# Optimization experiments

Measured on AMD Instinct MI355X. Metric: run time of the kernel, lower is better.

Reference implementation:

```python
import jax, jax.numpy as jnp
import numpy as np

DIM = 4096
N_HEADS = 32
HEAD_DIM = DIM // N_HEADS
BSZ = 4
SEQLEN = 512
MAX_SEQ = 2048
NEG = -1e9


def _qlinear(x, q, s):
    # int-quantized weight [out,in] dequantized with per-output-channel scale
    w = q.astype(jnp.float32) * s[:, None]
    return jnp.einsum('bsd,od->bso', x, w)


def _apply_rotary(xq, xk, cos, sin):
    # xq,xk: [b,s,h,hd]; cos,sin: [s,hd/2]
    def rot(t):
        b, s, h, d = t.shape
        t = t.reshape(b, s, h, d // 2, 2)
        tr, ti = t[..., 0], t[..., 1]
        c = cos[None, :, None, :]
        sn = sin[None, :, None, :]
        out_r = tr * c - ti * sn
        out_i = tr * sn + ti * c
        return jnp.stack([out_r, out_i], axis=-1).reshape(b, s, h, d)
    return rot(xq), rot(xk)


def setup_inputs() -> dict:
    key = jax.random.key(0)
    ks = jax.random.split(key, 12)
    x = jax.random.normal(ks[0], (BSZ, SEQLEN, DIM), dtype=jnp.float32)
    inv = 1.0 / (10000.0 ** (jnp.arange(0, HEAD_DIM, 2, dtype=jnp.float32) / HEAD_DIM))
    ang = jnp.arange(SEQLEN, dtype=jnp.float32)[:, None] * inv[None, :]
    freqs_cos, freqs_sin = jnp.cos(ang), jnp.sin(ang)
    input_idexes = jnp.arange(SEQLEN, dtype=jnp.int32)  # cache slots being written
    # causal additive mask over full cache: query at position i may attend j <= i
    j = jnp.arange(MAX_SEQ)
    mask = jnp.where(j[None, :] <= input_idexes[:, None], 0.0, NEG).astype(jnp.float32)
    mask = mask[None, None]  # [1,1,S,MAX_SEQ]
    cache_k = jnp.zeros((BSZ, MAX_SEQ, N_HEADS, HEAD_DIM), jnp.float32)
    cache_v = jnp.zeros((BSZ, MAX_SEQ, N_HEADS, HEAD_DIM), jnp.float32)
    SCALE = 2.0 / (127.0 * np.sqrt(DIM))
    def mkw(kq, kscale):
        q = jax.random.randint(kq, (DIM, DIM), -127, 128, dtype=jnp.int32)
        s = jax.random.uniform(kscale, (DIM,), dtype=jnp.float32) * SCALE
        return q, s
    wq_q, wq_s = mkw(ks[1], ks[2])
    wk_q, wk_s = mkw(ks[3], ks[4])
    wv_q, wv_s = mkw(ks[5], ks[6])
    wo_q, wo_s = mkw(ks[7], ks[8])
    return dict(x=x, freqs_cos=freqs_cos, freqs_sin=freqs_sin, mask=mask,
                input_idexes=input_idexes, cache_k=cache_k, cache_v=cache_v,
                wq_q=wq_q, wq_s=wq_s, wk_q=wk_q, wk_s=wk_s,
                wv_q=wv_q, wv_s=wv_s, wo_q=wo_q, wo_s=wo_s)


def reference(x, freqs_cos, freqs_sin, mask, input_idexes, cache_k, cache_v,
              wq_q, wq_s, wk_q, wk_s, wv_q, wv_s, wo_q, wo_s):
    bsz, seqlen, _ = x.shape
    xq = _qlinear(x, wq_q, wq_s).reshape(bsz, seqlen, N_HEADS, HEAD_DIM)
    xk = _qlinear(x, wk_q, wk_s).reshape(bsz, seqlen, N_HEADS, HEAD_DIM)
    xv = _qlinear(x, wv_q, wv_s).reshape(bsz, seqlen, N_HEADS, HEAD_DIM)
    xq, xk = _apply_rotary(xq, xk, freqs_cos, freqs_sin)
    # KV-cache append (index_copy on dim 1)
    cache_k = cache_k.at[:, input_idexes].set(xk)
    cache_v = cache_v.at[:, input_idexes].set(xv)
    # [b,h,q,d] x [b,h,k,d] -> [b,h,q,k]
    scores = jnp.einsum('bqhd,bkhd->bhqk', xq, cache_k) / np.sqrt(HEAD_DIM)
    scores = scores + mask
    probs = jax.nn.softmax(scores.astype(jnp.float32), axis=-1).astype(xq.dtype)
    out = jnp.einsum('bhqk,bkhd->bqhd', probs, cache_v).reshape(bsz, seqlen, -1)
    out = _qlinear(out, wo_q, wo_s)
    return out, (cache_k, cache_v)
```

## Files before the change

### kernel.cpp

```cpp
#include <hip/hip_runtime.h>
#include <cstdint>
#include <cstddef>

typedef __bf16 bf16;
typedef __attribute__((ext_vector_type(8))) __bf16 bf16x8;
typedef __attribute__((ext_vector_type(2))) __bf16 bf16x2;
typedef __attribute__((ext_vector_type(4))) float f32x4;
typedef __attribute__((ext_vector_type(2))) float f32x2;
typedef __attribute__((ext_vector_type(4))) int i32x4;

#define DIMN 4096
#define SEQ 512
#define MAXSEQ 2048
#define NHEAD 32
#define HD 128
#define NBH 128
#define MTOK 2048

#define BM 128
#define BN 128
#define BK 32
#define BKI 128

__device__ __forceinline__ void gld_lds16(const void* g, void* l) {
  __builtin_amdgcn_global_load_lds(
      (const __attribute__((address_space(1))) unsigned int*)g,
      (__attribute__((address_space(3))) unsigned int*)l, 16, 0, 0);
}

__device__ __forceinline__ void gemm_core(const bf16* Ablk, const bf16* Bblk,
                                          int lda, int ldb, int kmax,
                                          f32x4 acc[4][4], bf16* As, bf16* Bs) {
  const int tid = threadIdx.x;
  const int wave = tid >> 6;
  const int lane = tid & 63;
  const int wm = (wave >> 1) * 64;
  const int wn = (wave & 1) * 64;
  const int lrow = lane & 15;
  const int lkq8 = (lane >> 4) * 8;
  const int srow = wave * 32 + (lane >> 2);
  const int scol = (lane & 3) * 8;
  const bf16* Ag = Ablk + (size_t)srow * lda + scol;
  const bf16* Bg = Bblk + (size_t)srow * ldb + scol;
  bf16* lA = As + wave * 32 * BK;
  bf16* lB = Bs + wave * 32 * BK;

  for (int k0 = 0; k0 < kmax; k0 += BK) {
    __syncthreads();
    gld_lds16(Ag + k0, lA);
    gld_lds16(Ag + k0 + (size_t)16 * lda, lA + 16 * BK);
    gld_lds16(Bg + k0, lB);
    gld_lds16(Bg + k0 + (size_t)16 * ldb, lB + 16 * BK);
    __syncthreads();
    bf16x8 a[4], b[4];
#pragma unroll
    for (int i = 0; i < 4; ++i)
      a[i] = *(const bf16x8*)(As + (wm + i * 16 + lrow) * BK + lkq8);
#pragma unroll
    for (int i = 0; i < 4; ++i)
      b[i] = *(const bf16x8*)(Bs + (wn + i * 16 + lrow) * BK + lkq8);
#pragma unroll
    for (int mi = 0; mi < 4; ++mi)
#pragma unroll
      for (int ni = 0; ni < 4; ++ni)
        acc[mi][ni] = __builtin_amdgcn_mfma_f32_16x16x32_bf16(a[mi], b[ni], acc[mi][ni], 0, 0, 0);
  }
}

__device__ __forceinline__ void gemm_core_i8(const char* Ablk, const char* Bblk,
                                             int lda, int ldb, int kmax,
                                             i32x4 acc[4][4], char* As, char* Bs) {
  const int tid = threadIdx.x;
  const int wave = tid >> 6;
  const int lane = tid & 63;
  const int wm = (wave >> 1) * 64;
  const int wn = (wave & 1) * 64;
  const int lrow = lane & 15;
  const int q = lane >> 4;
  const int srow = wave * 32 + (lane >> 3);
  const int scol = (((lane & 7) ^ ((lane >> 3) & 7)) * 16);
  const char* Ag = Ablk + (size_t)srow * lda + scol;
  const char* Bg = Bblk + (size_t)srow * ldb + scol;
  char* lA = As + wave * 32 * BKI;
  char* lB = Bs + wave * 32 * BKI;

  for (int k0 = 0; k0 < kmax; k0 += BKI) {
    __syncthreads();
#pragma unroll
    for (int r = 0; r < 4; ++r) {
      gld_lds16(Ag + k0 + (size_t)(8 * r) * lda, lA + 8 * r * BKI);
      gld_lds16(Bg + k0 + (size_t)(8 * r) * ldb, lB + 8 * r * BKI);
    }
    __syncthreads();
#pragma unroll
    for (int kk = 0; kk < 2; ++kk) {
      i32x4 a[4], b[4];
#pragma unroll
      for (int i = 0; i < 4; ++i) {
        const int row = wm + i * 16 + lrow;
        const int slot = (kk * 4 + q) ^ (lrow & 7);
        a[i] = *(const i32x4*)(As + row * BKI + slot * 16);
      }
#pragma unroll
      for (int i = 0; i < 4; ++i) {
        const int row = wn + i * 16 + lrow;
        const int slot = (kk * 4 + q) ^ (lrow & 7);
        b[i] = *(const i32x4*)(Bs + row * BKI + slot * 16);
      }
#pragma unroll
      for (int mi = 0; mi < 4; ++mi)
#pragma unroll
        for (int ni = 0; ni < 4; ++ni)
          acc[mi][ni] = __builtin_amdgcn_mfma_i32_16x16x64_i8(a[mi], b[ni], acc[mi][ni], 0, 0, 0);
    }
  }
}

#define ACC_INIT_F(acc)                                 \
  f32x4 acc[4][4];                                      \
  _Pragma("unroll") for (int _i = 0; _i < 4; ++_i)      \
      _Pragma("unroll") for (int _j = 0; _j < 4; ++_j)  \
          acc[_i][_j] = f32x4{0.f, 0.f, 0.f, 0.f};

#define ACC_INIT_I(acc)                                 \
  i32x4 acc[4][4];                                      \
  _Pragma("unroll") for (int _i = 0; _i < 4; ++_i)      \
      _Pragma("unroll") for (int _j = 0; _j < 4; ++_j)  \
          acc[_i][_j] = i32x4{0, 0, 0, 0};

#define EPI_COORDS                                      \
  const int lane = threadIdx.x & 63;                    \
  const int wave = threadIdx.x >> 6;                    \
  const int wm = (wave >> 1) * 64, wn = (wave & 1) * 64;\
  const int cq = (lane >> 4) * 4, cc = lane & 15;

__global__ __launch_bounds__(256) void k_prep(
    const int* __restrict__ q0, const int* __restrict__ q1,
    const int* __restrict__ q2, const int* __restrict__ q3,
    char* __restrict__ w8, const float* __restrict__ x,
    char* __restrict__ x8, float* __restrict__ xs,
    float* __restrict__ ck, float* __restrict__ cv) {
  __shared__ float red[4];
  const int bx = blockIdx.x;
  const int tid = threadIdx.x;
  if (bx < 16384) {
    const int w = bx >> 12;
    const int* q = (w == 0) ? q0 : (w == 1) ? q1 : (w == 2) ? q2 : q3;
    char* wp = w8 + (size_t)w * 16777216ull;
    size_t i = ((size_t)(bx & 4095) * 256 + tid) * 16;
    const i32x4* qp = (const i32x4*)(q + i);
    i32x4 a = qp[0], b = qp[1], c = qp[2], d = qp[3];
    i32x4 o;
    o[0] = (a[0] & 255) | ((a[1] & 255) << 8) | ((a[2] & 255) << 16) | (a[3] << 24);
    o[1] = (b[0] & 255) | ((b[1] & 255) << 8) | ((b[2] & 255) << 16) | (b[3] << 24);
    o[2] = (c[0] & 255) | ((c[1] & 255) << 8) | ((c[2] & 255) << 16) | (c[3] << 24);
    o[3] = (d[0] & 255) | ((d[1] & 255) << 8) | ((d[2] & 255) << 16) | (d[3] << 24);
    *(i32x4*)(wp + i) = o;
  } else if (bx < 18432) {
    const int row = bx - 16384;
    const float* src = x + (size_t)row * DIMN + tid * 16;
    f32x4 v[4];
#pragma unroll
    for (int j = 0; j < 4; ++j) v[j] = ((const f32x4*)src)[j];
    float am = 0.f;
#pragma unroll
    for (int j = 0; j < 4; ++j)
#pragma unroll
      for (int e = 0; e < 4; ++e) am = fmaxf(am, fabsf(v[j][e]));
#pragma unroll
    for (int off = 32; off; off >>= 1) am = fmaxf(am, __shfl_xor(am, off, 64));
    if ((tid & 63) == 0) red[tid >> 6] = am;
    __syncthreads();
    am = fmaxf(fmaxf(red[0], red[1]), fmaxf(red[2], red[3]));
    const float inv = am > 0.f ? 127.f / am : 0.f;
    i32x4 o;
#pragma unroll
    for (int j = 0; j < 4; ++j) {
      int b0 = (int)rintf(v[j][0] * inv), b1 = (int)rintf(v[j][1] * inv);
      int b2 = (int)rintf(v[j][2] * inv), b3 = (int)rintf(v[j][3] * inv);
      o[j] = (b0 & 255) | ((b1 & 255) << 8) | ((b2 & 255) << 16) | (b3 << 24);
    }
    *(i32x4*)(x8 + (size_t)row * DIMN + tid * 16) = o;
    if (tid == 0) xs[row] = am * (1.f / 127.f);
  } else {
    const int z = bx - 18432;
    const int region = z / 6144;
    const int zoff = z - region * 6144;
    const int b = region >> 1;
    float* base = (region & 1) ? cv : ck;
    char* p = (char*)(base + ((size_t)b * MAXSEQ + SEQ) * DIMN);
    *(f32x4*)(p + (size_t)zoff * 4096 + tid * 16) = f32x4{0.f, 0.f, 0.f, 0.f};
  }
}

__global__ __launch_bounds__(256) void k_quant_attn(const bf16* __restrict__ at,
                                                    char* __restrict__ a8,
                                                    float* __restrict__ as_) {
  __shared__ float red[4];
  const int row = blockIdx.x, tid = threadIdx.x;
  const bf16* src = at + (size_t)row * DIMN + tid * 16;
  bf16x8 h0 = ((const bf16x8*)src)[0], h1 = ((const bf16x8*)src)[1];
  float f[16];
#pragma unroll
  for (int j = 0; j < 8; ++j) { f[j] = (float)h0[j]; f[8 + j] = (float)h1[j]; }
  float am = 0.f;
#pragma unroll
  for (int j = 0; j < 16; ++j) am = fmaxf(am, fabsf(f[j]));
#pragma unroll
  for (int off = 32; off; off >>= 1) am = fmaxf(am, __shfl_xor(am, off, 64));
  if ((tid & 63) == 0) red[tid >> 6] = am;
  __syncthreads();
  am = fmaxf(fmaxf(red[0], red[1]), fmaxf(red[2], red[3]));
  const float inv = am > 0.f ? 127.f / am : 0.f;
  i32x4 o;
#pragma unroll
  for (int j = 0; j < 4; ++j) {
    int b0 = (int)rintf(f[j * 4 + 0] * inv), b1 = (int)rintf(f[j * 4 + 1] * inv);
    int b2 = (int)rintf(f[j * 4 + 2] * inv), b3 = (int)rintf(f[j * 4 + 3] * inv);
    o[j] = (b0 & 255) | ((b1 & 255) << 8) | ((b2 & 255) << 16) | (b3 << 24);
  }
  *(i32x4*)(a8 + (size_t)row * DIMN + tid * 16) = o;
  if (tid == 0) as_[row] = am * (1.f / 127.f);
}

__global__ __launch_bounds__(256, 2) void k_gemm_qkv8(
    const char* __restrict__ X8, const char* __restrict__ W8,
    const float* __restrict__ xs, const float* __restrict__ sq,
    const float* __restrict__ sk, const float* __restrict__ sv,
    const float* __restrict__ fc, const float* __restrict__ fs,
    const int* __restrict__ idx, bf16* __restrict__ qbf,
    bf16* __restrict__ kbf, float* __restrict__ ck, float* __restrict__ cv) {
  __shared__ __align__(16) char As[BM * BKI];
  __shared__ __align__(16) char Bs[BN * BKI];
  const int n0 = blockIdx.x * BN;
  const int m0 = blockIdx.y * BM;
  const int z = blockIdx.z;
  const char* W = W8 + (size_t)z * 16777216ull;
  const float* sw = (z == 0) ? sq : (z == 1) ? sk : sv;
  ACC_INIT_I(acc);
  gemm_core_i8(X8 + (size_t)m0 * DIMN, W + (size_t)n0 * DIMN, DIMN, DIMN, DIMN, acc, As, Bs);
  EPI_COORDS;
  if (z < 2) {
    bf16* dst = (z == 0) ? qbf : kbf;
#pragma unroll
    for (int mi = 0; mi < 4; ++mi)
#pragma unroll
      for (int ni = 0; ni < 4; ++ni)
#pragma unroll
        for (int r = 0; r < 4; ++r) {
          const int row = m0 + wm + mi * 16 + cq + r;
          const int col = n0 + wn + ni * 16 + cc;
          const float v = (float)acc[mi][ni][r] * xs[row] * sw[col];
          const float pv = __shfl_xor(v, 1, 64);
          const int s = row & 511, b = row >> 9;
          const int hd = col & 127, h = col >> 7;
          const int d2 = hd >> 1;
          const float c = fc[s * 64 + d2], sn = fs[s * 64 + d2];
          const float o = (col & 1) ? (pv * sn + v * c) : (v * c - pv * sn);
          dst[(((size_t)(b * NHEAD + h)) * SEQ + s) * HD + hd] = (bf16)o;
          if (z == 1) {
            const int pos = idx[s];
            ck[((size_t)b * MAXSEQ + pos) * DIMN + col] = o;
          }
        }
  } else {
#pragma unroll
    for (int mi = 0; mi < 4; ++mi)
#pragma unroll
      for (int ni = 0; ni < 4; ++ni)
#pragma unroll
        for (int r = 0; r < 4; ++r) {
          const int row = m0 + wm + mi * 16 + cq + r;
          const int col = n0 + wn + ni * 16 + cc;
          const int s = row & 511, b = row >> 9;
          cv[((size_t)b * MAXSEQ + s) * DIMN + col] =
              (float)acc[mi][ni][r] * xs[row] * sw[col];
        }
  }
}

__global__ __launch_bounds__(256) void k_vt(const float* __restrict__ cv,
                                            bf16* __restrict__ vt) {
  __shared__ float tile[32][129];
  const int s0 = blockIdx.x * 32;
  const int bh = blockIdx.y;
  const int b = bh >> 5, h = bh & 31;
  const int tid = threadIdx.x;
  const float* src = cv + (size_t)b * MAXSEQ * DIMN + h * HD;
#pragma unroll
  for (int p = 0; p < 16; ++p) {
    const int row = p * 2 + (tid >> 7);
    const int d = tid & 127;
    tile[row][d] = src[(size_t)(s0 + row) * DIMN + d];
  }
  __syncthreads();
  bf16* dst = vt + (size_t)bh * HD * SEQ;
#pragma unroll
  for (int c = 0; c < 16; ++c) {
    const int d = c * 8 + (tid >> 5);
    const int sl = tid & 31;
    dst[(size_t)d * SEQ + s0 + sl] = (bf16)tile[sl][d];
  }
}

__constant__ int g_tm[10] = {0, 1, 1, 2, 2, 2, 3, 3, 3, 3};
__constant__ int g_tn[10] = {0, 0, 1, 0, 1, 2, 0, 1, 2, 3};

__global__ __launch_bounds__(256, 2) void k_gemm_qk(
    const bf16* __restrict__ qb, const bf16* __restrict__ kb,
    bf16* __restrict__ sc) {
  const int m0 = g_tm[blockIdx.x] * BM;
  const int n0 = g_tn[blockIdx.x] * BN;
  const int bh = blockIdx.z;
  __shared__ __align__(16) bf16 As[BM * BK];
  __shared__ __align__(16) bf16 Bs[BN * BK];
  ACC_INIT_F(acc);
  gemm_core(qb + (size_t)bh * SEQ * HD + (size_t)m0 * HD,
            kb + (size_t)bh * SEQ * HD + (size_t)n0 * HD, HD, HD, HD, acc, As, Bs);
  EPI_COORDS;
  bf16* dst = sc + (size_t)bh * SEQ * SEQ;
#pragma unroll
  for (int mi = 0; mi < 4; ++mi)
#pragma unroll
    for (int ni = 0; ni < 4; ++ni)
#pragma unroll
      for (int r = 0; r < 4; ++r) {
        const int row = m0 + wm + mi * 16 + cq + r;
        const int col = n0 + wn + ni * 16 + cc;
        dst[(size_t)row * SEQ + col] = (bf16)(acc[mi][ni][r] * 0.08838834764831845f);
      }
}

__global__ __launch_bounds__(256) void k_softmax(bf16* __restrict__ sc) {
  const int row = blockIdx.x * 4 + (threadIdx.x >> 6);
  const int lane = threadIdx.x & 63;
  const int q = row & 511;
  bf16* p = sc + (size_t)row * SEQ + lane * 8;
  bf16x8 v8 = *(const bf16x8*)p;
  float lv[8];
  float m = -3.0e38f;
#pragma unroll
  for (int j = 0; j < 8; ++j) {
    const int kj = lane * 8 + j;
    lv[j] = (kj <= q) ? (float)v8[j] : -3.0e38f;
    m = fmaxf(m, lv[j]);
  }
#pragma unroll
  for (int off = 32; off; off >>= 1) m = fmaxf(m, __shfl_xor(m, off, 64));
  float e[8];
  float sum = 0.f;
#pragma unroll
  for (int j = 0; j < 8; ++j) {
    e[j] = (lane * 8 + j <= q) ? __expf(lv[j] - m) : 0.f;
    sum += e[j];
  }
#pragma unroll
  for (int off = 32; off; off >>= 1) sum += __shfl_xor(sum, off, 64);
  const float r = 1.f / sum;
  bf16x8 o;
#pragma unroll
  for (int j = 0; j < 8; ++j) o[j] = (bf16)(e[j] * r);
  *(bf16x8*)p = o;
}

__global__ __launch_bounds__(256, 2) void k_gemm_pv(
    const bf16* __restrict__ P, const bf16* __restrict__ vt,
    bf16* __restrict__ attn) {
  const int m0 = blockIdx.y * BM;
  const int bh = blockIdx.z;
  const int kmax = m0 + BM;
  __shared__ __align__(16) bf16 As[BM * BK];
  __shared__ __align__(16) bf16 Bs[BN * BK];
  ACC_INIT_F(acc);
  gemm_core(P + (size_t)bh * SEQ * SEQ + (size_t)m0 * SEQ,
            vt + (size_t)bh * HD * SEQ, SEQ, SEQ, kmax, acc, As, Bs);
  EPI_COORDS;
  const int b = bh >> 5, h = bh & 31;
#pragma unroll
  for (int mi = 0; mi < 4; ++mi)
#pragma unroll
    for (int ni = 0; ni < 4; ++ni)
#pragma unroll
      for (int r = 0; r < 4; ++r) {
        const int row = m0 + wm + mi * 16 + cq + r;
        const int col = wn + ni * 16 + cc;
        attn[((size_t)(b * SEQ + row)) * DIMN + h * HD + col] = (bf16)acc[mi][ni][r];
      }
}

__global__ __launch_bounds__(256, 2) void k_gemm_out8(
    const char* __restrict__ A8, const char* __restrict__ WO8,
    const float* __restrict__ as_, const float* __restrict__ so,
    float* __restrict__ out) {
  __shared__ __align__(16) char As[BM * BKI];
  __shared__ __align__(16) char Bs[BN * BKI];
  const int n0 = blockIdx.x * BN;
  const int m0 = blockIdx.y * BM;
  ACC_INIT_I(acc);
  gemm_core_i8(A8 + (size_t)m0 * DIMN, WO8 + (size_t)n0 * DIMN, DIMN, DIMN, DIMN, acc, As, Bs);
  EPI_COORDS;
#pragma unroll
  for (int mi = 0; mi < 4; ++mi)
#pragma unroll
    for (int ni = 0; ni < 4; ++ni)
#pragma unroll
      for (int r = 0; r < 4; ++r) {
        const int row = m0 + wm + mi * 16 + cq + r;
        const int col = n0 + wn + ni * 16 + cc;
        out[(size_t)row * DIMN + col] = (float)acc[mi][ni][r] * as_[row] * so[col];
      }
}

extern "C" void kernel_launch(void* const* d_in, const int* in_sizes, int n_in,
                              void* d_out, int out_size, void* d_ws, size_t ws_size,
                              hipStream_t stream) {
  const float* x = (const float*)d_in[0];
  const float* fc = (const float*)d_in[1];
  const float* fs = (const float*)d_in[2];
  const int* idx = (const int*)d_in[4];
  const int* wq_q = (const int*)d_in[7];
  const int* wk_q = (const int*)d_in[9];
  const int* wv_q = (const int*)d_in[11];
  const int* wo_q = (const int*)d_in[13];
  const float* wq_s = (const float*)d_in[8];
  const float* wk_s = (const float*)d_in[10];
  const float* wv_s = (const float*)d_in[12];
  const float* wo_s = (const float*)d_in[14];

  float* out = (float*)d_out;
  float* ck_out = out + 8388608;
  float* cv_out = ck_out + 33554432;

  char* ws = (char*)d_ws;
  char* W8   = ws;
  char* X8   = ws + 67108864ull;
  float* XS  = (float*)(ws + 75497472ull);
  float* AS  = (float*)(ws + 75513856ull);
  bf16* QBF  = (bf16*)(ws + 83886080ull);
  bf16* KBF  = (bf16*)(ws + 100663296ull);
  bf16* VTB  = (bf16*)(ws + 117440512ull);
  bf16* ATTN = (bf16*)(ws + 134217728ull);
  char* A8   = ws + 150994944ull;
  bf16* SC   = (bf16*)(ws + 167772160ull);

  k_prep<<<dim3(67584), 256, 0, stream>>>(wq_q, wk_q, wv_q, wo_q, W8, x, X8, XS,
                                          ck_out, cv_out);
  k_gemm_qkv8<<<dim3(32, 16, 3), 256, 0, stream>>>(
      X8, W8, XS, wq_s, wk_s, wv_s, fc, fs, idx, QBF, KBF, ck_out, cv_out);
  k_vt<<<dim3(16, 128), 256, 0, stream>>>(cv_out, VTB);
  k_gemm_qk<<<dim3(10, 1, 128), 256, 0, stream>>>(QBF, KBF, SC);
  k_softmax<<<dim3(16384), 256, 0, stream>>>(SC);
  k_gemm_pv<<<dim3(1, 4, 128), 256, 0, stream>>>(SC, VTB, ATTN);
  k_quant_attn<<<dim3(2048), 256, 0, stream>>>(ATTN, A8, AS);
  k_gemm_out8<<<dim3(32, 16), 256, 0, stream>>>(A8, W8 + 50331648ull, AS, wo_s, out);
  (void)in_sizes; (void)n_in; (void)out_size; (void)ws_size;
}
```

Baseline: 871.9 us.

## Rewrite int8 GEMM core as 256x256 double-buffered pipelined tile with 8 waves

Replaces the 128x128 int8 GEMM core with a 256x256 block tile run by 512 threads, using a 128KB double-buffered LDS layout with a swizzle. Global-to-LDS loads for the next k-tiles are interleaved with MFMA groups, separated by explicit barriers, scheduler barriers, waitcnt and setprio hints. The aim is to hide load latency and raise operand reuse per block in both the QKV and output projections. In exchange the grids shrink to 384 and 128 blocks, which may leave CUs idle, especially for the output projection. The pipeline also prefetches k-tiles past the end of each row.

```diff
diff --git a/kernel.cpp b/kernel.cpp
--- a/kernel.cpp
+++ b/kernel.cpp
@@ -20,7 +20,6 @@
 #define BM 128
 #define BN 128
 #define BK 32
-#define BKI 128
 
 __device__ __forceinline__ void gld_lds16(const void* g, void* l) {
   __builtin_amdgcn_global_load_lds(
@@ -67,52 +66,92 @@
   }
 }
 
-__device__ __forceinline__ void gemm_core_i8(const char* Ablk, const char* Bblk,
-                                             int lda, int ldb, int kmax,
-                                             i32x4 acc[4][4], char* As, char* Bs) {
+
+#define PBAR do {                              \
+    asm volatile("" ::: "memory");             \
+    __builtin_amdgcn_sched_barrier(0);         \
+    __builtin_amdgcn_s_barrier();              \
+    __builtin_amdgcn_sched_barrier(0);         \
+    asm volatile("" ::: "memory");             \
+  } while (0)
+
+#define STG_A(KT, H, LB) do {                                    \
+    const char* _g = Asrc + (KT) * 128 + (H) * 64;               \
+    char* _l = (LB) + (H) * 16384 + sdst;                        \
+    gld_lds16(_g, _l);                                           \
+    gld_lds16(_g + (size_t)128 * DIMN, _l + 8192);               \
+  } while (0)
+#define STG_B(KT, H, LB) do {                                    \
+    const char* _g = Bsrc + (KT) * 128 + (H) * 64;               \
+    char* _l = (LB) + 32768 + (H) * 16384 + sdst;                \
+    gld_lds16(_g, _l);                                           \
+    gld_lds16(_g + (size_t)128 * DIMN, _l + 8192);               \
+  } while (0)
+
+#define LDA8(DST, MI, H, LB) \
+  DST = *(const i32x4*)((LB) + (H) * 16384 + (MI) * 1024 + aoff)
+#define LDB8(DST, NI, H, LB) \
+  DST = *(const i32x4*)((LB) + (H) * 16384 + (NI) * 1024 + boff)
+
+#define MFMA16(G)                                                           \
+    __builtin_amdgcn_s_setprio(1);                                          \
+    _Pragma("unroll") for (int _i = 0; _i < 4; ++_i)                        \
+      _Pragma("unroll") for (int _n = 0; _n < 4; ++_n)                      \
+        acc[(G) * 4 + _i][_n] = __builtin_amdgcn_mfma_i32_16x16x64_i8(      \
+            a[_i], b[_n], acc[(G) * 4 + _i][_n], 0, 0, 0);                  \
+    __builtin_amdgcn_s_setprio(0)
+
+#define TILE8(T, CUR, OTH) do {                                             \
+    i32x4 a[4], b[4];                                                       \
+                                              \
+    _Pragma("unroll") for (int n = 0; n < 4; ++n) LDB8(b[n], n, 0, CUR);    \
+    _Pragma("unroll") for (int i = 0; i < 4; ++i) LDA8(a[i], i, 0, CUR);    \
+    STG_A((T) + 1, 1, OTH);                                                 \
+    PBAR; MFMA16(0); PBAR;                                                  \
+                                              \
+    _Pragma("unroll") for (int i = 0; i < 4; ++i) LDA8(a[i], 4 + i, 0, CUR);\
+    STG_B((T) + 1, 1, OTH);                                                 \
+    PBAR; MFMA16(1); PBAR;                                                  \
+                                              \
+    _Pragma("unroll") for (int n = 0; n < 4; ++n) LDB8(b[n], n, 1, CUR);    \
+    _Pragma("unroll") for (int i = 0; i < 4; ++i) LDA8(a[i], i, 1, CUR);    \
+    STG_A((T) + 2, 0, CUR);                                                 \
+    PBAR; MFMA16(0); PBAR;                                                  \
+                                              \
+    _Pragma("unroll") for (int i = 0; i < 4; ++i) LDA8(a[i], 4 + i, 1, CUR);\
+    STG_B((T) + 2, 0, CUR);                                                 \
+    asm volatile("s_waitcnt vmcnt(4)" ::: "memory");                        \
+    PBAR; MFMA16(1); PBAR;                                                  \
+  } while (0)
+
+__device__ __forceinline__ void gemm256_i8(const char* __restrict__ Ablk,
+                                           const char* __restrict__ Bblk,
+                                           char* lds, i32x4 acc[8][4]) {
   const int tid = threadIdx.x;
-  const int wave = tid >> 6;
-  const int lane = tid & 63;
-  const int wm = (wave >> 1) * 64;
-  const int wn = (wave & 1) * 64;
-  const int lrow = lane & 15;
-  const int q = lane >> 4;
-  const int srow = wave * 32 + (lane >> 3);
-  const int scol = (((lane & 7) ^ ((lane >> 3) & 7)) * 16);
-  const char* Ag = Ablk + (size_t)srow * lda + scol;
-  const char* Bg = Bblk + (size_t)srow * ldb + scol;
-  char* lA = As + wave * 32 * BKI;
-  char* lB = Bs + wave * 32 * BKI;
-
-  for (int k0 = 0; k0 < kmax; k0 += BKI) {
-    __syncthreads();
-#pragma unroll
-    for (int r = 0; r < 4; ++r) {
-      gld_lds16(Ag + k0 + (size_t)(8 * r) * lda, lA + 8 * r * BKI);
-      gld_lds16(Bg + k0 + (size_t)(8 * r) * ldb, lB + 8 * r * BKI);
-    }
-    __syncthreads();
-#pragma unroll
-    for (int kk = 0; kk < 2; ++kk) {
-      i32x4 a[4], b[4];
-#pragma unroll
-      for (int i = 0; i < 4; ++i) {
-        const int row = wm + i * 16 + lrow;
-        const int slot = (kk * 4 + q) ^ (lrow & 7);
-        a[i] = *(const i32x4*)(As + row * BKI + slot * 16);
-      }
-#pragma unroll
-      for (int i = 0; i < 4; ++i) {
-        const int row = wn + i * 16 + lrow;
-        const int slot = (kk * 4 + q) ^ (lrow & 7);
-        b[i] = *(const i32x4*)(Bs + row * BKI + slot * 16);
-      }
-#pragma unroll
-      for (int mi = 0; mi < 4; ++mi)
-#pragma unroll
-        for (int ni = 0; ni < 4; ++ni)
-          acc[mi][ni] = __builtin_amdgcn_mfma_i32_16x16x64_i8(a[mi], b[ni], acc[mi][ni], 0, 0, 0);
-    }
+  const int wave = tid >> 6, lane = tid & 63;
+  const int wm = (wave >> 2) * 128, wn = (wave & 3) * 64;
+  const int lrow = lane & 15, q = lane >> 4;
+  const int swz = ((q ^ (lrow & 3)) << 4);
+  const int aoff = (wm + lrow) * 64 + swz;
+  const int boff = 32768 + (wn + lrow) * 64 + swz;
+  const int gsw = ((lane & 3) ^ ((lane >> 2) & 3)) << 4;
+  const char* Asrc = Ablk + (size_t)(wave * 16 + (lane >> 2)) * DIMN + gsw;
+  const char* Bsrc = Bblk + (size_t)(wave * 16 + (lane >> 2)) * DIMN + gsw;
+  const int sdst = wave * 1024;
+  char* const L0 = lds;
+  char* const L1 = lds + 65536;
+
+  STG_A(0, 0, L0); STG_B(0, 0, L0);
+  STG_A(0, 1, L0); STG_B(0, 1, L0);
+  STG_A(1, 0, L1); STG_B(1, 0, L1);
+  asm volatile("s_waitcnt vmcnt(4)" ::: "memory");
+  __builtin_amdgcn_sched_barrier(0);
+  __builtin_amdgcn_s_barrier();
+  __builtin_amdgcn_sched_barrier(0);
+
+  for (int t = 0; t < DIMN / 128; t += 2) {
+    TILE8(t, L0, L1);
+    TILE8(t + 1, L1, L0);
   }
 }
 
@@ -122,9 +161,9 @@
       _Pragma("unroll") for (int _j = 0; _j < 4; ++_j)  \
           acc[_i][_j] = f32x4{0.f, 0.f, 0.f, 0.f};
 
-#define ACC_INIT_I(acc)                                 \
-  i32x4 acc[4][4];                                      \
-  _Pragma("unroll") for (int _i = 0; _i < 4; ++_i)      \
+#define ACC_INIT_I8(acc)                                \
+  i32x4 acc[8][4];                                      \
+  _Pragma("unroll") for (int _i = 0; _i < 8; ++_i)      \
       _Pragma("unroll") for (int _j = 0; _j < 4; ++_j)  \
           acc[_i][_j] = i32x4{0, 0, 0, 0};
 
@@ -132,6 +171,12 @@
   const int lane = threadIdx.x & 63;                    \
   const int wave = threadIdx.x >> 6;                    \
   const int wm = (wave >> 1) * 64, wn = (wave & 1) * 64;\
+  const int cq = (lane >> 4) * 4, cc = lane & 15;
+
+#define EPI8_COORDS                                       \
+  const int lane = threadIdx.x & 63;                      \
+  const int wave = threadIdx.x >> 6;                      \
+  const int wm = (wave >> 2) * 128, wn = (wave & 3) * 64; \
   const int cq = (lane >> 4) * 4, cc = lane & 15;
 
 __global__ __launch_bounds__(256) void k_prep(
@@ -223,27 +268,26 @@
   if (tid == 0) as_[row] = am * (1.f / 127.f);
 }
 
-__global__ __launch_bounds__(256, 2) void k_gemm_qkv8(
+__global__ __launch_bounds__(512, 2) void k_gemm_qkv8(
     const char* __restrict__ X8, const char* __restrict__ W8,
     const float* __restrict__ xs, const float* __restrict__ sq,
     const float* __restrict__ sk, const float* __restrict__ sv,
     const float* __restrict__ fc, const float* __restrict__ fs,
     const int* __restrict__ idx, bf16* __restrict__ qbf,
     bf16* __restrict__ kbf, float* __restrict__ ck, float* __restrict__ cv) {
-  __shared__ __align__(16) char As[BM * BKI];
-  __shared__ __align__(16) char Bs[BN * BKI];
-  const int n0 = blockIdx.x * BN;
-  const int m0 = blockIdx.y * BM;
+  __shared__ __align__(16) char lds[131072];
+  const int n0 = blockIdx.x * 256;
+  const int m0 = blockIdx.y * 256;
   const int z = blockIdx.z;
   const char* W = W8 + (size_t)z * 16777216ull;
   const float* sw = (z == 0) ? sq : (z == 1) ? sk : sv;
-  ACC_INIT_I(acc);
-  gemm_core_i8(X8 + (size_t)m0 * DIMN, W + (size_t)n0 * DIMN, DIMN, DIMN, DIMN, acc, As, Bs);
-  EPI_COORDS;
+  ACC_INIT_I8(acc);
+  gemm256_i8(X8 + (size_t)m0 * DIMN, W + (size_t)n0 * DIMN, lds, acc);
+  EPI8_COORDS;
   if (z < 2) {
     bf16* dst = (z == 0) ? qbf : kbf;
 #pragma unroll
-    for (int mi = 0; mi < 4; ++mi)
+    for (int mi = 0; mi < 8; ++mi)
 #pragma unroll
       for (int ni = 0; ni < 4; ++ni)
 #pragma unroll
@@ -265,7 +309,7 @@
         }
   } else {
 #pragma unroll
-    for (int mi = 0; mi < 4; ++mi)
+    for (int mi = 0; mi < 8; ++mi)
 #pragma unroll
       for (int ni = 0; ni < 4; ++ni)
 #pragma unroll
@@ -388,19 +432,18 @@
       }
 }
 
-__global__ __launch_bounds__(256, 2) void k_gemm_out8(
+__global__ __launch_bounds__(512, 2) void k_gemm_out8(
     const char* __restrict__ A8, const char* __restrict__ WO8,
     const float* __restrict__ as_, const float* __restrict__ so,
     float* __restrict__ out) {
-  __shared__ __align__(16) char As[BM * BKI];
-  __shared__ __align__(16) char Bs[BN * BKI];
-  const int n0 = blockIdx.x * BN;
-  const int m0 = blockIdx.y * BM;
-  ACC_INIT_I(acc);
-  gemm_core_i8(A8 + (size_t)m0 * DIMN, WO8 + (size_t)n0 * DIMN, DIMN, DIMN, DIMN, acc, As, Bs);
-  EPI_COORDS;
-#pragma unroll
-  for (int mi = 0; mi < 4; ++mi)
+  __shared__ __align__(16) char lds[131072];
+  const int n0 = blockIdx.x * 256;
+  const int m0 = blockIdx.y * 256;
+  ACC_INIT_I8(acc);
+  gemm256_i8(A8 + (size_t)m0 * DIMN, WO8 + (size_t)n0 * DIMN, lds, acc);
+  EPI8_COORDS;
+#pragma unroll
+  for (int mi = 0; mi < 8; ++mi)
 #pragma unroll
     for (int ni = 0; ni < 4; ++ni)
 #pragma unroll
@@ -445,13 +488,13 @@
 
   k_prep<<<dim3(67584), 256, 0, stream>>>(wq_q, wk_q, wv_q, wo_q, W8, x, X8, XS,
                                           ck_out, cv_out);
-  k_gemm_qkv8<<<dim3(32, 16, 3), 256, 0, stream>>>(
+  k_gemm_qkv8<<<dim3(16, 8, 3), 512, 0, stream>>>(
       X8, W8, XS, wq_s, wk_s, wv_s, fc, fs, idx, QBF, KBF, ck_out, cv_out);
   k_vt<<<dim3(16, 128), 256, 0, stream>>>(cv_out, VTB);
   k_gemm_qk<<<dim3(10, 1, 128), 256, 0, stream>>>(QBF, KBF, SC);
   k_softmax<<<dim3(16384), 256, 0, stream>>>(SC);
   k_gemm_pv<<<dim3(1, 4, 128), 256, 0, stream>>>(SC, VTB, ATTN);
   k_quant_attn<<<dim3(2048), 256, 0, stream>>>(ATTN, A8, AS);
-  k_gemm_out8<<<dim3(32, 16), 256, 0, stream>>>(A8, W8 + 50331648ull, AS, wo_s, out);
+  k_gemm_out8<<<dim3(16, 8), 512, 0, stream>>>(A8, W8 + 50331648ull, AS, wo_s, out);
   (void)in_sizes; (void)n_in; (void)out_size; (void)ws_size;
 }
```

New measurement: 904.6 us. 1.04x slower.
